# Kernel optimization log

Measured on AMD Instinct MI355X. Metric: run time of the kernel, lower is better.

## Reference

```python
import jax, jax.numpy as jnp
import numpy as np

_EPS = 1e-6
_ZCA_EPS = 1e-5
NEG_SLOPE_ATTN = 0.2   # LeakyReLU inside score_mlp
NEG_SLOPE_FFN = 0.1    # VNLinearLeakyReLU negative_slope


def _safe_norm(x, axis, keepdims=False):
    # norm with zero-gradient at exactly-zero vectors (matches torch subgradient)
    sq = jnp.sum(x * x, axis=axis, keepdims=keepdims)
    safe = jnp.where(sq == 0, 1.0, sq)
    return jnp.sqrt(safe) * (sq > 0)


def vn_linear(W, x):
    # W: (out, in); x: (B, C_in, 3, N) -> (B, C_out, 3, N)
    return jnp.einsum('oi,bivn->bovn', W, x)


def zca_layernorm(x, gamma):
    # x: (B, C, 3, N); whiten the 3D vector components per batch element
    B, C = x.shape[0], x.shape[1]
    xf = x.reshape(B, C, 3, -1).transpose(0, 2, 1, 3).reshape(B, 3, -1)
    xf = xf.astype(jnp.float32)
    mu = xf.mean(axis=-1, keepdims=True)
    xc = xf - mu
    M = xc.shape[-1]
    cov = (xc @ xc.transpose(0, 2, 1)) / (float(M) + _EPS)  # (B,3,3)
    cov = cov + _ZCA_EPS * jnp.eye(3, dtype=cov.dtype)[None]
    w, V = jnp.linalg.eigh(cov)
    w = jnp.maximum(w, _ZCA_EPS)
    Wm = (V * jax.lax.rsqrt(w)[:, None, :]) @ V.transpose(0, 2, 1)  # (B,3,3)
    xw = Wm @ xc
    xw = xw.reshape(B, 3, C, -1).transpose(0, 2, 1, 3).reshape(x.shape).astype(x.dtype)
    return xw * gamma[None, :, None, None]


def cwsa_attention(x, pos, Wq, Wk, Wv, Wo, W1, b1, W2, b2):
    q = vn_linear(Wq, x)  # (B,C,3,N)
    k = vn_linear(Wk, x)
    v = vn_linear(Wv, x)
    qk = q.transpose(0, 3, 1, 2)  # (B,N,C,3)
    kk = k.transpose(0, 3, 1, 2)
    vv = v.transpose(0, 3, 1, 2)
    rel = qk[:, :, None, :, :] - kk[:, None, :, :, :]      # (B,N,N,C,3)
    rel_norm = _safe_norm(rel, axis=-1)                    # (B,N,N,C)
    rel_mean = rel_norm.mean(axis=-1, keepdims=True)       # (B,N,N,1)
    rel_pos = pos[:, :, None, :] - pos[:, None, :, :]      # (B,N,N,3)
    rel_pos_norm = _safe_norm(rel_pos, axis=-1, keepdims=True)  # (B,N,N,1)
    score_in = jnp.concatenate([rel_mean, rel_pos_norm], axis=-1)  # (B,N,N,2)
    h = jax.nn.leaky_relu(score_in @ W1.T + b1, NEG_SLOPE_ATTN)
    scores = h @ W2.T + b2                                  # (B,N,N,C)
    attn = jax.nn.softmax(scores, axis=2)                   # softmax over keys j
    out = jnp.einsum('bijk,bjkd->bikd', attn, vv)           # (B,N,C,3)
    out = out.transpose(0, 2, 3, 1)                         # (B,C,3,N)
    return vn_linear(Wo, out)


def vn_leaky_relu(p, d, ns):
    # p, d: (B, C, 3, N)
    dot = jnp.sum(p * d, axis=2, keepdims=True)
    dsq = jnp.sum(d * d, axis=2, keepdims=True)
    mask = (dot >= 0).astype(p.dtype)
    proj = p - (dot / (dsq + _EPS)) * d
    return ns * p + (1.0 - ns) * (mask * p + (1.0 - mask) * proj)


def ffn(x, Wfeat, Wdir, Wffn2):
    p = vn_linear(Wfeat, x)
    d = vn_linear(Wdir, x)
    h = vn_leaky_relu(p, d, NEG_SLOPE_FFN)
    return vn_linear(Wffn2, h)


def setup_inputs() -> dict:
    key = jax.random.key(0)
    ks = jax.random.split(key, 16)
    B, C, N = 2, 128, 256
    hidden, ratio = 64, 2
    sC = 1.0 / np.sqrt(C)
    inp = {
        'x': jax.random.normal(ks[0], (B, C, 3, N), dtype=jnp.float32),
        'pos': jax.random.normal(ks[1], (B, N, 3), dtype=jnp.float32),
        'Wq': jax.random.normal(ks[2], (C, C), dtype=jnp.float32) * sC,
        'Wk': jax.random.normal(ks[3], (C, C), dtype=jnp.float32) * sC,
        'Wv': jax.random.normal(ks[4], (C, C), dtype=jnp.float32) * sC,
        'Wo': jax.random.normal(ks[5], (C, C), dtype=jnp.float32) * sC,
        'W1': jax.random.normal(ks[6], (hidden, 2), dtype=jnp.float32) * (1.0 / np.sqrt(2.0)),
        'b1': jnp.zeros((hidden,), dtype=jnp.float32),
        'W2': jax.random.normal(ks[7], (C, hidden), dtype=jnp.float32) * (1.0 / np.sqrt(hidden)),
        'b2': jnp.zeros((C,), dtype=jnp.float32),
        'gamma1': jnp.ones((C,), dtype=jnp.float32),
        'Wfeat': jax.random.normal(ks[8], (C * ratio, C), dtype=jnp.float32) * sC,
        'Wdir': jax.random.normal(ks[9], (C * ratio, C), dtype=jnp.float32) * sC,
        'Wffn2': jax.random.normal(ks[10], (C, C * ratio), dtype=jnp.float32) * (1.0 / np.sqrt(C * ratio)),
        'gamma2': jnp.ones((C,), dtype=jnp.float32),
    }
    return inp


def reference(x, pos, Wq, Wk, Wv, Wo, W1, b1, W2, b2, gamma1, Wfeat, Wdir, Wffn2, gamma2):
    a = cwsa_attention(x, pos, Wq, Wk, Wv, Wo, W1, b1, W2, b2)
    x1 = zca_layernorm(x + a, gamma1)
    f = ffn(x1, Wfeat, Wdir, Wffn2)
    return zca_layernorm(x1 + f, gamma2)
```

## Files before the change

### kernel.cpp

```cpp
#include <hip/hip_runtime.h>
#include <math.h>

#define BB 2
#define CC 128
#define NN 256
#define HH 64
#define CHX 256
#define COLS 768
#define NEG_ATTN 0.2f
#define NEG_FFN 0.1f

typedef __attribute__((ext_vector_type(8))) short short8b;
typedef __attribute__((ext_vector_type(4))) float f32x4;

__device__ __forceinline__ unsigned bf16rne(float x) {
  unsigned u = __float_as_uint(x);
  return (u + 0x7fffu + ((u >> 16) & 1u)) >> 16;
}

__global__ __launch_bounds__(256) void k_qkv(
    const float* __restrict__ x, const float* __restrict__ Wq,
    const float* __restrict__ Wk, const float* __restrict__ Wv,
    float* __restrict__ q_t, float* __restrict__ k_nat, float* __restrict__ v_t)
{
  const int ct = blockIdx.x, b = blockIdx.z;
  const int which = blockIdx.y >> 1, cohalf = blockIdx.y & 1;
  const int col0 = ct * 32, co0 = cohalf * 64;
  const int t = threadIdx.x;
  __shared__ __align__(16) float xt[CC][32];
  __shared__ float Wl[64][33];
  const float* xb = x + (size_t)b * CC * COLS;
  for (int idx = t; idx < CC * 32; idx += 256) {
    int r = idx >> 5, cc = idx & 31;
    xt[r][cc] = xb[r * COLS + col0 + cc];
  }
  const float* W = (which == 0) ? Wq : ((which == 1) ? Wk : Wv);
  const int cop = t >> 3;
  const int colq = t & 7;
  float acc[2][4];
#pragma unroll
  for (int r = 0; r < 2; r++)
#pragma unroll
    for (int k = 0; k < 4; k++) acc[r][k] = 0.f;
  for (int cu = 0; cu < 4; cu++) {
    __syncthreads();
    for (int idx = t; idx < 64 * 32; idx += 256) {
      int row = idx >> 5, ci = idx & 31;
      Wl[row][ci] = W[(size_t)(co0 + row) * CC + cu * 32 + ci];
    }
    __syncthreads();
#pragma unroll 8
    for (int ci = 0; ci < 32; ci++) {
      float w0 = Wl[cop * 2][ci], w1 = Wl[cop * 2 + 1][ci];
      const float4 xv = *(reinterpret_cast<const float4*>(xt[cu * 32 + ci]) + colq);
      acc[0][0] = fmaf(w0, xv.x, acc[0][0]); acc[0][1] = fmaf(w0, xv.y, acc[0][1]);
      acc[0][2] = fmaf(w0, xv.z, acc[0][2]); acc[0][3] = fmaf(w0, xv.w, acc[0][3]);
      acc[1][0] = fmaf(w1, xv.x, acc[1][0]); acc[1][1] = fmaf(w1, xv.y, acc[1][1]);
      acc[1][2] = fmaf(w1, xv.z, acc[1][2]); acc[1][3] = fmaf(w1, xv.w, acc[1][3]);
    }
  }
#pragma unroll
  for (int r = 0; r < 2; r++) {
    const int co_g = co0 + cop * 2 + r;
    if (which == 1) {
      float4 o = {acc[r][0], acc[r][1], acc[r][2], acc[r][3]};
      *reinterpret_cast<float4*>(&k_nat[(size_t)(b * CC + co_g) * COLS + col0 + colq * 4]) = o;
    } else {
#pragma unroll
      for (int k = 0; k < 4; k++) {
        int col = col0 + colq * 4 + k;
        int v = col >> 8, n = col & 255;
        if (which == 0) q_t[((size_t)(b * NN + n) * CC + co_g) * 3 + v] = acc[r][k];
        else            v_t[((size_t)(b * NN + n) * 3 + v) * CC + co_g] = acc[r][k];
      }
    }
  }
}

__global__ __launch_bounds__(256) void k_rel(
    const float* __restrict__ q_t, const float* __restrict__ k_nat,
    const float* __restrict__ pos, float* __restrict__ rm_all,
    float* __restrict__ rp_all)
{
  const int i = blockIdx.x, b = blockIdx.y;
  const int t = threadIdx.x;
  __shared__ float qv[CC * 3];
  for (int idx = t; idx < CC * 3; idx += 256)
    qv[idx] = q_t[(size_t)(b * NN + i) * CC * 3 + idx];
  __syncthreads();
  const int j = t;
  const float* kb = k_nat + (size_t)b * CC * COLS;
  float p0 = 0.f, p1 = 0.f, p2 = 0.f, p3 = 0.f;
  for (int c = 0; c < CC; c += 4) {
    float kx0 = kb[(c + 0) * COLS + j], ky0 = kb[(c + 0) * COLS + 256 + j], kz0 = kb[(c + 0) * COLS + 512 + j];
    float kx1 = kb[(c + 1) * COLS + j], ky1 = kb[(c + 1) * COLS + 256 + j], kz1 = kb[(c + 1) * COLS + 512 + j];
    float kx2 = kb[(c + 2) * COLS + j], ky2 = kb[(c + 2) * COLS + 256 + j], kz2 = kb[(c + 2) * COLS + 512 + j];
    float kx3 = kb[(c + 3) * COLS + j], ky3 = kb[(c + 3) * COLS + 256 + j], kz3 = kb[(c + 3) * COLS + 512 + j];
    float dx, dy, dz, sq;
    dx = kx0 - qv[(c + 0) * 3]; dy = ky0 - qv[(c + 0) * 3 + 1]; dz = kz0 - qv[(c + 0) * 3 + 2];
    sq = dx * dx + dy * dy + dz * dz; p0 += (sq > 0.f) ? sqrtf(sq) : 0.f;
    dx = kx1 - qv[(c + 1) * 3]; dy = ky1 - qv[(c + 1) * 3 + 1]; dz = kz1 - qv[(c + 1) * 3 + 2];
    sq = dx * dx + dy * dy + dz * dz; p1 += (sq > 0.f) ? sqrtf(sq) : 0.f;
    dx = kx2 - qv[(c + 2) * 3]; dy = ky2 - qv[(c + 2) * 3 + 1]; dz = kz2 - qv[(c + 2) * 3 + 2];
    sq = dx * dx + dy * dy + dz * dz; p2 += (sq > 0.f) ? sqrtf(sq) : 0.f;
    dx = kx3 - qv[(c + 3) * 3]; dy = ky3 - qv[(c + 3) * 3 + 1]; dz = kz3 - qv[(c + 3) * 3 + 2];
    sq = dx * dx + dy * dy + dz * dz; p3 += (sq > 0.f) ? sqrtf(sq) : 0.f;
  }
  rm_all[(size_t)(b * NN + i) * NN + j] = ((p0 + p1) + (p2 + p3)) * (1.f / 128.f);
  float dx = pos[(b * NN + i) * 3 + 0] - pos[(b * NN + j) * 3 + 0];
  float dy = pos[(b * NN + i) * 3 + 1] - pos[(b * NN + j) * 3 + 1];
  float dz = pos[(b * NN + i) * 3 + 2] - pos[(b * NN + j) * 3 + 2];
  float sq = dx * dx + dy * dy + dz * dz;
  rp_all[(size_t)(b * NN + i) * NN + j] = (sq > 0.f) ? sqrtf(sq) : 0.f;
}

__global__ __launch_bounds__(256, 4) void k_attn(
    const float* __restrict__ rm_all, const float* __restrict__ rp_all,
    const float* __restrict__ v_t, const float* __restrict__ W1,
    const float* __restrict__ b1, const float* __restrict__ W2,
    float* __restrict__ a_nat)
{
  const int i = blockIdx.x, chalf = blockIdx.y, b = blockIdx.z;
  const int t = threadIdx.x;
  __shared__ __align__(16) short hh_s[64 * 64];
  __shared__ __align__(16) short w2_s[64 * 64];
  __shared__ float sc_s[64 * 65];
  __shared__ float rm_s[NN], rp_s[NN];

  rm_s[t] = rm_all[(size_t)(b * NN + i) * NN + t];
  rp_s[t] = rp_all[(size_t)(b * NN + i) * NN + t];
  {
    const int cl = t >> 2, h0 = (t & 3) * 16;
    const float* wrow = W2 + (size_t)(chalf * 64 + cl) * HH + h0;
#pragma unroll
    for (int e = 0; e < 8; e++) {
      unsigned lo = bf16rne(wrow[2 * e]);
      unsigned hi = bf16rne(wrow[2 * e + 1]);
      int didx = (cl * 32 + (h0 >> 1) + e) ^ ((cl & 7) << 2);
      ((unsigned*)w2_s)[didx] = lo | (hi << 16);
    }
  }
  const int h2 = (t & 31) * 2, jgrp = t >> 5;
  const float4 w1v = *reinterpret_cast<const float4*>(W1 + 2 * h2);
  const float c0 = b1[h2], c1 = b1[h2 + 1];
  __syncthreads();

  auto phase2 = [&](int q) {
#pragma unroll
    for (int jj = 0; jj < 8; jj++) {
      int jl = jgrp * 8 + jj;
      int jg = q * 64 + jl;
      float rmv = rm_s[jg], rpv = rp_s[jg];
      float g0 = fmaf(w1v.x, rmv, fmaf(w1v.y, rpv, c0));
      float g1 = fmaf(w1v.z, rmv, fmaf(w1v.w, rpv, c1));
      g0 = (g0 >= 0.f) ? g0 : NEG_ATTN * g0;
      g1 = (g1 >= 0.f) ? g1 : NEG_ATTN * g1;
      int didx = (jl * 32 + (h2 >> 1)) ^ ((jl & 7) << 2);
      ((unsigned*)hh_s)[didx] = bf16rne(g0) | (bf16rne(g1) << 16);
    }
  };

  phase2(0);
  __syncthreads();

  const int lane = t & 63, wv = t >> 6;
  const int g8 = (lane >> 4) * 8;
  const int cdx = wv * 16 + (lane & 15);
  const short8b bfr0 = *reinterpret_cast<const short8b*>(&w2_s[(cdx * 64 + g8) ^ ((cdx & 7) << 3)]);
  const short8b bfr1 = *reinterpret_cast<const short8b*>(&w2_s[(cdx * 64 + 32 + g8) ^ ((cdx & 7) << 3)]);

  const int cl = lane;
  const int par = wv;
  const int vc = chalf * 64 + cl;
  float l = 0.f, a0 = 0.f, a1 = 0.f, a2 = 0.f;

  for (int q = 0; q < 4; q++) {
#pragma unroll
    for (int jt = 0; jt < 4; jt++) {
      int jr = jt * 16 + (lane & 15);
      short8b af0 = *reinterpret_cast<const short8b*>(&hh_s[(jr * 64 + g8) ^ ((jr & 7) << 3)]);
      short8b af1 = *reinterpret_cast<const short8b*>(&hh_s[(jr * 64 + 32 + g8) ^ ((jr & 7) << 3)]);
      f32x4 acc = {0.f, 0.f, 0.f, 0.f};
      acc = __builtin_amdgcn_mfma_f32_16x16x32_bf16(af0, bfr0, acc, 0, 0, 0);
      acc = __builtin_amdgcn_mfma_f32_16x16x32_bf16(af1, bfr1, acc, 0, 0, 0);
      int row0 = jt * 16 + (lane >> 4) * 4;
      int ccol = wv * 16 + (lane & 15);
#pragma unroll
      for (int r = 0; r < 4; r++) sc_s[(row0 + r) * 65 + ccol] = acc[r];
    }
    __syncthreads();
#pragma unroll
    for (int jj = 0; jj < 16; jj++) {
      int jl = jj * 4 + par;
      int jg = q * 64 + jl;
      float s = sc_s[jl * 65 + cl];
      const float* vb = v_t + ((size_t)(b * NN + jg) * 3) * CC + vc;
      float v0 = vb[0], v1 = vb[CC], v2 = vb[2 * CC];
      float p = __expf(s);
      l += p;
      a0 = fmaf(p, v0, a0);
      a1 = fmaf(p, v1, a1);
      a2 = fmaf(p, v2, a2);
    }
    if (q < 3) phase2(q + 1);
    __syncthreads();
  }

  float* mrg = sc_s;
  if (par != 0) {
    float* mp = mrg + (cl * 3 + (par - 1)) * 4;
    mp[0] = l; mp[1] = a0; mp[2] = a1; mp[3] = a2;
  }
  __syncthreads();
  if (par == 0) {
    float L = l, A0 = a0, A1 = a1, A2 = a2;
#pragma unroll
    for (int q = 0; q < 3; q++) {
      const float* mp = mrg + (cl * 3 + q) * 4;
      L += mp[0]; A0 += mp[1]; A1 += mp[2]; A2 += mp[3];
    }
    float inv = 1.f / L;
    float* ap = a_nat + (size_t)(b * CC + vc) * COLS + i;
    ap[0] = A0 * inv; ap[256] = A1 * inv; ap[512] = A2 * inv;
  }
}

__global__ __launch_bounds__(256) void k_wo_res(
    const float* __restrict__ a_nat, const float* __restrict__ Wo,
    const float* __restrict__ x, float* __restrict__ y1)
{
  const int ct = blockIdx.x, cohalf = blockIdx.y, b = blockIdx.z;
  const int col0 = ct * 16, co0 = cohalf * 64;
  const int t = threadIdx.x;
  __shared__ __align__(16) float at[CC][16];
  __shared__ float Wl[64][33];
  const float* ab = a_nat + (size_t)b * CC * COLS;
  for (int idx = t; idx < CC * 16; idx += 256) {
    int r = idx >> 4, cc = idx & 15;
    at[r][cc] = ab[r * COLS + col0 + cc];
  }
  const int cop = t >> 3, colp = t & 7;
  float acc[2][2] = {{0.f, 0.f}, {0.f, 0.f}};
  for (int cu = 0; cu < 4; cu++) {
    __syncthreads();
    for (int idx = t; idx < 64 * 32; idx += 256) {
      int row = idx >> 5, ci = idx & 31;
      Wl[row][ci] = Wo[(size_t)(co0 + row) * CC + cu * 32 + ci];
    }
    __syncthreads();
#pragma unroll 8
    for (int ci = 0; ci < 32; ci++) {
      float w0 = Wl[cop * 2][ci], w1 = Wl[cop * 2 + 1][ci];
      const float2 xv = *(reinterpret_cast<const float2*>(at[cu * 32 + ci]) + colp);
      acc[0][0] = fmaf(w0, xv.x, acc[0][0]); acc[0][1] = fmaf(w0, xv.y, acc[0][1]);
      acc[1][0] = fmaf(w1, xv.x, acc[1][0]); acc[1][1] = fmaf(w1, xv.y, acc[1][1]);
    }
  }
#pragma unroll
  for (int r = 0; r < 2; r++) {
    const size_t base = (size_t)(b * CC + co0 + cop * 2 + r) * COLS + col0 + colp * 2;
    y1[base]     = x[base]     + acc[r][0];
    y1[base + 1] = x[base + 1] + acc[r][1];
  }
}

__global__ __launch_bounds__(1024) void k_stats(
    const float* __restrict__ y, float* __restrict__ stats)
{
  const int b = blockIdx.x;
  const float* yb = y + (size_t)b * CC * COLS;
  const int t = threadIdx.x;
  float v9[9];
#pragma unroll
  for (int k = 0; k < 9; k++) v9[k] = 0.f;
  for (int e = 0; e < 32; e++) {
    int idx = e * 1024 + t;
    int cidx = idx >> 8, n = idx & 255;
    const float* row = yb + cidx * COLS + n;
    float v0 = row[0], v1 = row[256], v2 = row[512];
    v9[0] += v0; v9[1] += v1; v9[2] += v2;
    v9[3] += v0 * v0; v9[4] += v0 * v1; v9[5] += v0 * v2;
    v9[6] += v1 * v1; v9[7] += v1 * v2; v9[8] += v2 * v2;
  }
#pragma unroll
  for (int off = 32; off >= 1; off >>= 1)
#pragma unroll
    for (int k = 0; k < 9; k++) v9[k] += __shfl_down(v9[k], off);
  __shared__ float red[16][9];
  const int wid = t >> 6, lane = t & 63;
  if (lane == 0)
#pragma unroll
    for (int k = 0; k < 9; k++) red[wid][k] = v9[k];
  __syncthreads();
  if (t == 0) {
    float tot[9];
#pragma unroll
    for (int k = 0; k < 9; k++) tot[k] = 0.f;
    for (int w = 0; w < 16; w++)
#pragma unroll
      for (int k = 0; k < 9; k++) tot[k] += red[w][k];
    const float M = (float)(CC * NN);
    float mu0 = tot[0] / M, mu1 = tot[1] / M, mu2 = tot[2] / M;
    float A[3][3];
    A[0][0] = (tot[3] - M * mu0 * mu0) / M + 1e-5f;
    A[0][1] = A[1][0] = (tot[4] - M * mu0 * mu1) / M;
    A[0][2] = A[2][0] = (tot[5] - M * mu0 * mu2) / M;
    A[1][1] = (tot[6] - M * mu1 * mu1) / M + 1e-5f;
    A[1][2] = A[2][1] = (tot[7] - M * mu1 * mu2) / M;
    A[2][2] = (tot[8] - M * mu2 * mu2) / M + 1e-5f;
    float V[3][3] = {{1.f, 0.f, 0.f}, {0.f, 1.f, 0.f}, {0.f, 0.f, 1.f}};
    for (int sweep = 0; sweep < 10; sweep++) {
      for (int pi = 0; pi < 3; pi++) {
        const int p = (pi == 2) ? 1 : 0;
        const int q = (pi == 0) ? 1 : 2;
        float apq = A[p][q];
        if (fabsf(apq) < 1e-30f) continue;
        float theta = (A[q][q] - A[p][p]) / (2.f * apq);
        float tt = 1.f / (fabsf(theta) + sqrtf(theta * theta + 1.f));
        if (theta < 0.f) tt = -tt;
        float cr = 1.f / sqrtf(tt * tt + 1.f);
        float sr = tt * cr;
        float app = A[p][p], aqq = A[q][q];
        A[p][p] = app - tt * apq;
        A[q][q] = aqq + tt * apq;
        A[p][q] = A[q][p] = 0.f;
        const int r = 3 - p - q;
        float arp = A[r][p], arq = A[r][q];
        A[r][p] = A[p][r] = cr * arp - sr * arq;
        A[r][q] = A[q][r] = sr * arp + cr * arq;
        for (int rr = 0; rr < 3; rr++) {
          float vrp = V[rr][p], vrq = V[rr][q];
          V[rr][p] = cr * vrp - sr * vrq;
          V[rr][q] = sr * vrp + cr * vrq;
        }
      }
    }
    float rs[3];
#pragma unroll
    for (int k = 0; k < 3; k++) rs[k] = rsqrtf(fmaxf(A[k][k], 1e-5f));
    float* st = stats + b * 12;
    st[0] = mu0; st[1] = mu1; st[2] = mu2;
    for (int u = 0; u < 3; u++)
      for (int v = 0; v < 3; v++) {
        float acc = 0.f;
        for (int k = 0; k < 3; k++) acc += V[u][k] * rs[k] * V[v][k];
        st[3 + u * 3 + v] = acc;
      }
  }
}

__global__ __launch_bounds__(256) void k_ffn1(
    const float* __restrict__ y1, const float* __restrict__ stats,
    const float* __restrict__ gamma, const float* __restrict__ Wfeat,
    const float* __restrict__ Wdir, float* __restrict__ hout)
{
  const int nt = blockIdx.x, cs = blockIdx.y, b = blockIdx.z;
  const int n0 = nt * 8, co0 = cs * 32;
  const int t = threadIdx.x;
  __shared__ float xt[CC][24];
  __shared__ float Wfl[32][33], Wdl[32][33];
  const float* yb = y1 + (size_t)b * CC * COLS;
  const float* st = stats + b * 12;
  for (int idx = t; idx < CC * 8; idx += 256) {
    int ci = idx >> 3, nn = idx & 7;
    const float* row = yb + ci * COLS + n0 + nn;
    float d0 = row[0] - st[0], d1 = row[256] - st[1], d2 = row[512] - st[2];
    float g = gamma[ci];
    xt[ci][nn]      = g * (st[3] * d0 + st[4] * d1 + st[5] * d2);
    xt[ci][8 + nn]  = g * (st[6] * d0 + st[7] * d1 + st[8] * d2);
    xt[ci][16 + nn] = g * (st[9] * d0 + st[10] * d1 + st[11] * d2);
  }
  const int co = t >> 3, nn = t & 7;
  float p[3] = {0.f, 0.f, 0.f}, d[3] = {0.f, 0.f, 0.f};
  for (int cu = 0; cu < 4; cu++) {
    __syncthreads();
    for (int idx = t; idx < 2048; idx += 256) {
      int row = (idx & 1023) >> 5, ci = idx & 31;
      if (idx < 1024) Wfl[row][ci] = Wfeat[(size_t)(co0 + row) * CC + cu * 32 + ci];
      else            Wdl[row][ci] = Wdir[(size_t)(co0 + row) * CC + cu * 32 + ci];
    }
    __syncthreads();
#pragma unroll 8
    for (int ci = 0; ci < 32; ci++) {
      float wf = Wfl[co][ci], wd = Wdl[co][ci];
      const float* xr = xt[cu * 32 + ci];
      float x0 = xr[nn], x1 = xr[8 + nn], x2 = xr[16 + nn];
      p[0] = fmaf(wf, x0, p[0]); p[1] = fmaf(wf, x1, p[1]); p[2] = fmaf(wf, x2, p[2]);
      d[0] = fmaf(wd, x0, d[0]); d[1] = fmaf(wd, x1, d[1]); d[2] = fmaf(wd, x2, d[2]);
    }
  }
  float dot = p[0] * d[0] + p[1] * d[1] + p[2] * d[2];
  float dsq = d[0] * d[0] + d[1] * d[1] + d[2] * d[2];
  float coef = (dot >= 0.f) ? 0.f : (1.f - NEG_FFN) * dot / (dsq + 1e-6f);
  float* hb = hout + (size_t)(b * CHX + co0 + co) * COLS;
#pragma unroll
  for (int v = 0; v < 3; v++)
    hb[v * 256 + n0 + nn] = p[v] - coef * d[v];
}

__global__ __launch_bounds__(256) void k_ffn2(
    const float* __restrict__ h, const float* __restrict__ Wffn2,
    const float* __restrict__ y1, const float* __restrict__ stats,
    const float* __restrict__ gamma, float* __restrict__ x2)
{
  const int ct = blockIdx.x, cohalf = blockIdx.y, b = blockIdx.z;
  const int col0 = ct * 16, co0 = cohalf * 64;
  const int t = threadIdx.x;
  __shared__ __align__(16) float ht[CHX][16];
  __shared__ float Wl[64][33];
  const float* hb = h + (size_t)b * CHX * COLS;
  for (int idx = t; idx < CHX * 16; idx += 256) {
    int r = idx >> 4, cc = idx & 15;
    ht[r][cc] = hb[r * COLS + col0 + cc];
  }
  const int cop = t >> 3, colp = t & 7;
  float acc[2][2] = {{0.f, 0.f}, {0.f, 0.f}};
  for (int cu = 0; cu < 8; cu++) {
    __syncthreads();
    for (int idx = t; idx < 64 * 32; idx += 256) {
      int row = idx >> 5, ci = idx & 31;
      Wl[row][ci] = Wffn2[(size_t)(co0 + row) * CHX + cu * 32 + ci];
    }
    __syncthreads();
#pragma unroll 8
    for (int ci = 0; ci < 32; ci++) {
      float w0 = Wl[cop * 2][ci], w1 = Wl[cop * 2 + 1][ci];
      const float2 xv = *(reinterpret_cast<const float2*>(ht[cu * 32 + ci]) + colp);
      acc[0][0] = fmaf(w0, xv.x, acc[0][0]); acc[0][1] = fmaf(w0, xv.y, acc[0][1]);
      acc[1][0] = fmaf(w1, xv.x, acc[1][0]); acc[1][1] = fmaf(w1, xv.y, acc[1][1]);
    }
  }
  const int col_base = col0 + colp * 2;
  const int v = col_base >> 8, n = col_base & 255;
  const float* st = stats + b * 12;
  const float w0 = st[3 + v * 3 + 0], w1 = st[3 + v * 3 + 1], w2 = st[3 + v * 3 + 2];
#pragma unroll
  for (int r = 0; r < 2; r++) {
    const int co_g = co0 + cop * 2 + r;
    const float g = gamma[co_g];
    const float* yr = y1 + (size_t)(b * CC + co_g) * COLS + n;
    const size_t base = (size_t)(b * CC + co_g) * COLS + col_base;
#pragma unroll
    for (int k = 0; k < 2; k++) {
      float d0 = yr[k] - st[0], d1 = yr[256 + k] - st[1], d2 = yr[512 + k] - st[2];
      x2[base + k] = g * (w0 * d0 + w1 * d1 + w2 * d2) + acc[r][k];
    }
  }
}

__global__ __launch_bounds__(256) void k_zca_apply(
    const float* __restrict__ y, const float* __restrict__ stats,
    const float* __restrict__ gamma, float* __restrict__ out)
{
  int idx = blockIdx.x * blockDim.x + threadIdx.x;
  int b = idx >> 15, rem = idx & 32767;
  int cidx = rem >> 8, n = rem & 255;
  const float* st = stats + b * 12;
  const size_t base = (size_t)(b * CC + cidx) * COLS + n;
  float v0 = y[base] - st[0];
  float v1 = y[base + 256] - st[1];
  float v2 = y[base + 512] - st[2];
  float g = gamma[cidx];
  out[base]       = g * (st[3] * v0 + st[4] * v1 + st[5] * v2);
  out[base + 256] = g * (st[6] * v0 + st[7] * v1 + st[8] * v2);
  out[base + 512] = g * (st[9] * v0 + st[10] * v1 + st[11] * v2);
}

extern "C" void kernel_launch(void* const* d_in, const int* in_sizes, int n_in,
                              void* d_out, int out_size, void* d_ws, size_t ws_size,
                              hipStream_t stream)
{
  (void)in_sizes; (void)n_in; (void)out_size; (void)ws_size;
  const float* x      = (const float*)d_in[0];
  const float* pos    = (const float*)d_in[1];
  const float* Wq     = (const float*)d_in[2];
  const float* Wk     = (const float*)d_in[3];
  const float* Wv     = (const float*)d_in[4];
  const float* Wo     = (const float*)d_in[5];
  const float* W1     = (const float*)d_in[6];
  const float* b1     = (const float*)d_in[7];
  const float* W2     = (const float*)d_in[8];
  const float* gamma1 = (const float*)d_in[10];
  const float* Wfeat  = (const float*)d_in[11];
  const float* Wdir   = (const float*)d_in[12];
  const float* Wffn2  = (const float*)d_in[13];
  const float* gamma2 = (const float*)d_in[14];

  float* ws = (float*)d_ws;
  const size_t SZ = (size_t)BB * CC * 3 * NN;
  const size_t RMSZ = (size_t)BB * NN * NN;
  float* q_t    = ws;
  float* k_nat  = ws + SZ;
  float* v_t    = ws + 2 * SZ;
  float* rm_all = ws + 3 * SZ;
  float* rp_all = ws + 3 * SZ + RMSZ;
  float* a_nat  = ws;
  float* y1     = ws + SZ;
  float* hbuf   = ws + 2 * SZ;
  float* x2     = ws;
  float* stats1 = ws + 4 * SZ;
  float* stats2 = ws + 4 * SZ + 64;

  k_qkv<<<dim3(24, 6, BB), 256, 0, stream>>>(x, Wq, Wk, Wv, q_t, k_nat, v_t);
  k_rel<<<dim3(NN, BB), 256, 0, stream>>>(q_t, k_nat, pos, rm_all, rp_all);
  k_attn<<<dim3(NN, 2, BB), 256, 0, stream>>>(rm_all, rp_all, v_t, W1, b1, W2, a_nat);
  k_wo_res<<<dim3(48, 2, BB), 256, 0, stream>>>(a_nat, Wo, x, y1);
  k_stats<<<BB, 1024, 0, stream>>>(y1, stats1);
  k_ffn1<<<dim3(32, 8, BB), 256, 0, stream>>>(y1, stats1, gamma1, Wfeat, Wdir, hbuf);
  k_ffn2<<<dim3(48, 2, BB), 256, 0, stream>>>(hbuf, Wffn2, y1, stats1, gamma1, x2);
  k_stats<<<BB, 1024, 0, stream>>>(x2, stats2);
  k_zca_apply<<<256, 256, 0, stream>>>(x2, stats2, gamma2, (float*)d_out);
}
```

Before: 119.3 us.

## Reuse K across query pairs, consume MFMA scores in registers, split ZCA stats reduction

```diff
diff --git a/kernel.cpp b/kernel.cpp
--- a/kernel.cpp
+++ b/kernel.cpp
@@ -82,36 +82,47 @@
     const float* __restrict__ pos, float* __restrict__ rm_all,
     float* __restrict__ rp_all)
 {
-  const int i = blockIdx.x, b = blockIdx.y;
+  const int i0 = blockIdx.x * 2, b = blockIdx.y;
   const int t = threadIdx.x;
-  __shared__ float qv[CC * 3];
-  for (int idx = t; idx < CC * 3; idx += 256)
-    qv[idx] = q_t[(size_t)(b * NN + i) * CC * 3 + idx];
+  __shared__ float qv[2 * CC * 3];
+  for (int idx = t; idx < 2 * CC * 3; idx += 256)
+    qv[idx] = q_t[(size_t)(b * NN + i0) * CC * 3 + idx];
   __syncthreads();
   const int j = t;
   const float* kb = k_nat + (size_t)b * CC * COLS;
-  float p0 = 0.f, p1 = 0.f, p2 = 0.f, p3 = 0.f;
-  for (int c = 0; c < CC; c += 4) {
-    float kx0 = kb[(c + 0) * COLS + j], ky0 = kb[(c + 0) * COLS + 256 + j], kz0 = kb[(c + 0) * COLS + 512 + j];
+  float a00 = 0.f, a01 = 0.f, a10 = 0.f, a11 = 0.f;
+  for (int c = 0; c < CC; c += 2) {
+    float kx0 = kb[c * COLS + j], ky0 = kb[c * COLS + 256 + j], kz0 = kb[c * COLS + 512 + j];
     float kx1 = kb[(c + 1) * COLS + j], ky1 = kb[(c + 1) * COLS + 256 + j], kz1 = kb[(c + 1) * COLS + 512 + j];
-    float kx2 = kb[(c + 2) * COLS + j], ky2 = kb[(c + 2) * COLS + 256 + j], kz2 = kb[(c + 2) * COLS + 512 + j];
-    float kx3 = kb[(c + 3) * COLS + j], ky3 = kb[(c + 3) * COLS + 256 + j], kz3 = kb[(c + 3) * COLS + 512 + j];
-    float dx, dy, dz, sq;
-    dx = kx0 - qv[(c + 0) * 3]; dy = ky0 - qv[(c + 0) * 3 + 1]; dz = kz0 - qv[(c + 0) * 3 + 2];
-    sq = dx * dx + dy * dy + dz * dz; p0 += (sq > 0.f) ? sqrtf(sq) : 0.f;
-    dx = kx1 - qv[(c + 1) * 3]; dy = ky1 - qv[(c + 1) * 3 + 1]; dz = kz1 - qv[(c + 1) * 3 + 2];
-    sq = dx * dx + dy * dy + dz * dz; p1 += (sq > 0.f) ? sqrtf(sq) : 0.f;
-    dx = kx2 - qv[(c + 2) * 3]; dy = ky2 - qv[(c + 2) * 3 + 1]; dz = kz2 - qv[(c + 2) * 3 + 2];
-    sq = dx * dx + dy * dy + dz * dz; p2 += (sq > 0.f) ? sqrtf(sq) : 0.f;
-    dx = kx3 - qv[(c + 3) * 3]; dy = ky3 - qv[(c + 3) * 3 + 1]; dz = kz3 - qv[(c + 3) * 3 + 2];
-    sq = dx * dx + dy * dy + dz * dz; p3 += (sq > 0.f) ? sqrtf(sq) : 0.f;
-  }
-  rm_all[(size_t)(b * NN + i) * NN + j] = ((p0 + p1) + (p2 + p3)) * (1.f / 128.f);
-  float dx = pos[(b * NN + i) * 3 + 0] - pos[(b * NN + j) * 3 + 0];
-  float dy = pos[(b * NN + i) * 3 + 1] - pos[(b * NN + j) * 3 + 1];
-  float dz = pos[(b * NN + i) * 3 + 2] - pos[(b * NN + j) * 3 + 2];
-  float sq = dx * dx + dy * dy + dz * dz;
-  rp_all[(size_t)(b * NN + i) * NN + j] = (sq > 0.f) ? sqrtf(sq) : 0.f;
+    {
+      float dx = kx0 - qv[c * 3], dy = ky0 - qv[c * 3 + 1], dz = kz0 - qv[c * 3 + 2];
+      float sq = dx * dx + dy * dy + dz * dz;
+      a00 += (sq > 0.f) ? sqrtf(sq) : 0.f;
+      dx = kx1 - qv[(c + 1) * 3]; dy = ky1 - qv[(c + 1) * 3 + 1]; dz = kz1 - qv[(c + 1) * 3 + 2];
+      sq = dx * dx + dy * dy + dz * dz;
+      a01 += (sq > 0.f) ? sqrtf(sq) : 0.f;
+    }
+    {
+      const float* q1 = qv + CC * 3;
+      float dx = kx0 - q1[c * 3], dy = ky0 - q1[c * 3 + 1], dz = kz0 - q1[c * 3 + 2];
+      float sq = dx * dx + dy * dy + dz * dz;
+      a10 += (sq > 0.f) ? sqrtf(sq) : 0.f;
+      dx = kx1 - q1[(c + 1) * 3]; dy = ky1 - q1[(c + 1) * 3 + 1]; dz = kz1 - q1[(c + 1) * 3 + 2];
+      sq = dx * dx + dy * dy + dz * dz;
+      a11 += (sq > 0.f) ? sqrtf(sq) : 0.f;
+    }
+  }
+  rm_all[(size_t)(b * NN + i0) * NN + j]     = (a00 + a01) * (1.f / 128.f);
+  rm_all[(size_t)(b * NN + i0 + 1) * NN + j] = (a10 + a11) * (1.f / 128.f);
+  float pjx = pos[(b * NN + j) * 3], pjy = pos[(b * NN + j) * 3 + 1], pjz = pos[(b * NN + j) * 3 + 2];
+#pragma unroll
+  for (int ii = 0; ii < 2; ii++) {
+    float dx = pos[(b * NN + i0 + ii) * 3] - pjx;
+    float dy = pos[(b * NN + i0 + ii) * 3 + 1] - pjy;
+    float dz = pos[(b * NN + i0 + ii) * 3 + 2] - pjz;
+    float sq = dx * dx + dy * dy + dz * dz;
+    rp_all[(size_t)(b * NN + i0 + ii) * NN + j] = (sq > 0.f) ? sqrtf(sq) : 0.f;
+  }
 }
 
 __global__ __launch_bounds__(256, 4) void k_attn(
@@ -122,10 +133,10 @@
 {
   const int i = blockIdx.x, chalf = blockIdx.y, b = blockIdx.z;
   const int t = threadIdx.x;
-  __shared__ __align__(16) short hh_s[64 * 64];
+  __shared__ __align__(16) short hh_s[2][64 * 64];
   __shared__ __align__(16) short w2_s[64 * 64];
-  __shared__ float sc_s[64 * 65];
   __shared__ float rm_s[NN], rp_s[NN];
+  __shared__ float mrg[64][3][4];
 
   rm_s[t] = rm_all[(size_t)(b * NN + i) * NN + t];
   rp_s[t] = rp_all[(size_t)(b * NN + i) * NN + t];
@@ -143,9 +154,9 @@
   const int h2 = (t & 31) * 2, jgrp = t >> 5;
   const float4 w1v = *reinterpret_cast<const float4*>(W1 + 2 * h2);
   const float c0 = b1[h2], c1 = b1[h2 + 1];
-  __syncthreads();
 
   auto phase2 = [&](int q) {
+    unsigned* dst = (unsigned*)hh_s[q & 1];
 #pragma unroll
     for (int jj = 0; jj < 8; jj++) {
       int jl = jgrp * 8 + jj;
@@ -156,10 +167,11 @@
       g0 = (g0 >= 0.f) ? g0 : NEG_ATTN * g0;
       g1 = (g1 >= 0.f) ? g1 : NEG_ATTN * g1;
       int didx = (jl * 32 + (h2 >> 1)) ^ ((jl & 7) << 2);
-      ((unsigned*)hh_s)[didx] = bf16rne(g0) | (bf16rne(g1) << 16);
+      dst[didx] = bf16rne(g0) | (bf16rne(g1) << 16);
     }
   };
 
+  __syncthreads();
   phase2(0);
   __syncthreads();
 
@@ -169,54 +181,47 @@
   const short8b bfr0 = *reinterpret_cast<const short8b*>(&w2_s[(cdx * 64 + g8) ^ ((cdx & 7) << 3)]);
   const short8b bfr1 = *reinterpret_cast<const short8b*>(&w2_s[(cdx * 64 + 32 + g8) ^ ((cdx & 7) << 3)]);
 
-  const int cl = lane;
-  const int par = wv;
-  const int vc = chalf * 64 + cl;
+  const int vc = chalf * 64 + cdx;
+  const int jg4 = (lane >> 4) * 4;
   float l = 0.f, a0 = 0.f, a1 = 0.f, a2 = 0.f;
 
   for (int q = 0; q < 4; q++) {
+    const short* hb = hh_s[q & 1];
 #pragma unroll
     for (int jt = 0; jt < 4; jt++) {
       int jr = jt * 16 + (lane & 15);
-      short8b af0 = *reinterpret_cast<const short8b*>(&hh_s[(jr * 64 + g8) ^ ((jr & 7) << 3)]);
-      short8b af1 = *reinterpret_cast<const short8b*>(&hh_s[(jr * 64 + 32 + g8) ^ ((jr & 7) << 3)]);
+      short8b af0 = *reinterpret_cast<const short8b*>(&hb[(jr * 64 + g8) ^ ((jr & 7) << 3)]);
+      short8b af1 = *reinterpret_cast<const short8b*>(&hb[(jr * 64 + 32 + g8) ^ ((jr & 7) << 3)]);
       f32x4 acc = {0.f, 0.f, 0.f, 0.f};
       acc = __builtin_amdgcn_mfma_f32_16x16x32_bf16(af0, bfr0, acc, 0, 0, 0);
       acc = __builtin_amdgcn_mfma_f32_16x16x32_bf16(af1, bfr1, acc, 0, 0, 0);
-      int row0 = jt * 16 + (lane >> 4) * 4;
-      int ccol = wv * 16 + (lane & 15);
-#pragma unroll
-      for (int r = 0; r < 4; r++) sc_s[(row0 + r) * 65 + ccol] = acc[r];
-    }
-    __syncthreads();
-#pragma unroll
-    for (int jj = 0; jj < 16; jj++) {
-      int jl = jj * 4 + par;
-      int jg = q * 64 + jl;
-      float s = sc_s[jl * 65 + cl];
-      const float* vb = v_t + ((size_t)(b * NN + jg) * 3) * CC + vc;
-      float v0 = vb[0], v1 = vb[CC], v2 = vb[2 * CC];
-      float p = __expf(s);
-      l += p;
-      a0 = fmaf(p, v0, a0);
-      a1 = fmaf(p, v1, a1);
-      a2 = fmaf(p, v2, a2);
+      const int jbase = q * 64 + jt * 16 + jg4;
+#pragma unroll
+      for (int r = 0; r < 4; r++) {
+        float p = __expf(acc[r]);
+        const float* vb = v_t + ((size_t)(b * NN + jbase + r) * 3) * CC + vc;
+        l += p;
+        a0 = fmaf(p, vb[0], a0);
+        a1 = fmaf(p, vb[CC], a1);
+        a2 = fmaf(p, vb[2 * CC], a2);
+      }
     }
     if (q < 3) phase2(q + 1);
     __syncthreads();
   }
 
-  float* mrg = sc_s;
-  if (par != 0) {
-    float* mp = mrg + (cl * 3 + (par - 1)) * 4;
+  const int g = lane >> 4;
+  const int cslot = cdx;
+  if (g != 0) {
+    float* mp = &mrg[cslot][g - 1][0];
     mp[0] = l; mp[1] = a0; mp[2] = a1; mp[3] = a2;
   }
   __syncthreads();
-  if (par == 0) {
+  if (g == 0) {
     float L = l, A0 = a0, A1 = a1, A2 = a2;
 #pragma unroll
-    for (int q = 0; q < 3; q++) {
-      const float* mp = mrg + (cl * 3 + q) * 4;
+    for (int gg = 0; gg < 3; gg++) {
+      const float* mp = &mrg[cslot][gg][0];
       L += mp[0]; A0 += mp[1]; A1 += mp[2]; A2 += mp[3];
     }
     float inv = 1.f / L;
@@ -264,17 +269,17 @@
   }
 }
 
-__global__ __launch_bounds__(1024) void k_stats(
-    const float* __restrict__ y, float* __restrict__ stats)
-{
-  const int b = blockIdx.x;
+__global__ __launch_bounds__(256) void k_stats1(
+    const float* __restrict__ y, float* __restrict__ partials)
+{
+  const int blk = blockIdx.x, b = blockIdx.y;
   const float* yb = y + (size_t)b * CC * COLS;
-  const int t = threadIdx.x;
   float v9[9];
 #pragma unroll
   for (int k = 0; k < 9; k++) v9[k] = 0.f;
-  for (int e = 0; e < 32; e++) {
-    int idx = e * 1024 + t;
+#pragma unroll
+  for (int e = 0; e < 4; e++) {
+    int idx = blk * 1024 + e * 256 + threadIdx.x;
     int cidx = idx >> 8, n = idx & 255;
     const float* row = yb + cidx * COLS + n;
     float v0 = row[0], v1 = row[256], v2 = row[512];
@@ -286,67 +291,78 @@
   for (int off = 32; off >= 1; off >>= 1)
 #pragma unroll
     for (int k = 0; k < 9; k++) v9[k] += __shfl_down(v9[k], off);
-  __shared__ float red[16][9];
-  const int wid = t >> 6, lane = t & 63;
+  __shared__ float red[4][9];
+  const int wid = threadIdx.x >> 6, lane = threadIdx.x & 63;
   if (lane == 0)
 #pragma unroll
     for (int k = 0; k < 9; k++) red[wid][k] = v9[k];
   __syncthreads();
-  if (t == 0) {
-    float tot[9];
-#pragma unroll
-    for (int k = 0; k < 9; k++) tot[k] = 0.f;
-    for (int w = 0; w < 16; w++)
-#pragma unroll
-      for (int k = 0; k < 9; k++) tot[k] += red[w][k];
-    const float M = (float)(CC * NN);
-    float mu0 = tot[0] / M, mu1 = tot[1] / M, mu2 = tot[2] / M;
-    float A[3][3];
-    A[0][0] = (tot[3] - M * mu0 * mu0) / M + 1e-5f;
-    A[0][1] = A[1][0] = (tot[4] - M * mu0 * mu1) / M;
-    A[0][2] = A[2][0] = (tot[5] - M * mu0 * mu2) / M;
-    A[1][1] = (tot[6] - M * mu1 * mu1) / M + 1e-5f;
-    A[1][2] = A[2][1] = (tot[7] - M * mu1 * mu2) / M;
-    A[2][2] = (tot[8] - M * mu2 * mu2) / M + 1e-5f;
-    float V[3][3] = {{1.f, 0.f, 0.f}, {0.f, 1.f, 0.f}, {0.f, 0.f, 1.f}};
-    for (int sweep = 0; sweep < 10; sweep++) {
-      for (int pi = 0; pi < 3; pi++) {
-        const int p = (pi == 2) ? 1 : 0;
-        const int q = (pi == 0) ? 1 : 2;
-        float apq = A[p][q];
-        if (fabsf(apq) < 1e-30f) continue;
-        float theta = (A[q][q] - A[p][p]) / (2.f * apq);
-        float tt = 1.f / (fabsf(theta) + sqrtf(theta * theta + 1.f));
-        if (theta < 0.f) tt = -tt;
-        float cr = 1.f / sqrtf(tt * tt + 1.f);
-        float sr = tt * cr;
-        float app = A[p][p], aqq = A[q][q];
-        A[p][p] = app - tt * apq;
-        A[q][q] = aqq + tt * apq;
-        A[p][q] = A[q][p] = 0.f;
-        const int r = 3 - p - q;
-        float arp = A[r][p], arq = A[r][q];
-        A[r][p] = A[p][r] = cr * arp - sr * arq;
-        A[r][q] = A[q][r] = sr * arp + cr * arq;
-        for (int rr = 0; rr < 3; rr++) {
-          float vrp = V[rr][p], vrq = V[rr][q];
-          V[rr][p] = cr * vrp - sr * vrq;
-          V[rr][q] = sr * vrp + cr * vrq;
-        }
+  if (threadIdx.x == 0) {
+#pragma unroll
+    for (int k = 0; k < 9; k++)
+      partials[(size_t)(b * 32 + blk) * 9 + k] =
+          ((red[0][k] + red[1][k]) + (red[2][k] + red[3][k]));
+  }
+}
+
+__global__ __launch_bounds__(64) void k_zca_fin(
+    const float* __restrict__ partials, float* __restrict__ stats)
+{
+  const int b = blockIdx.x;
+  if (threadIdx.x != 0) return;
+  float tot[9];
+#pragma unroll
+  for (int k = 0; k < 9; k++) tot[k] = 0.f;
+  for (int p = 0; p < 32; p++)
+#pragma unroll
+    for (int k = 0; k < 9; k++) tot[k] += partials[(size_t)(b * 32 + p) * 9 + k];
+  const float M = (float)(CC * NN);
+  float mu0 = tot[0] / M, mu1 = tot[1] / M, mu2 = tot[2] / M;
+  float A[3][3];
+  A[0][0] = (tot[3] - M * mu0 * mu0) / M + 1e-5f;
+  A[0][1] = A[1][0] = (tot[4] - M * mu0 * mu1) / M;
+  A[0][2] = A[2][0] = (tot[5] - M * mu0 * mu2) / M;
+  A[1][1] = (tot[6] - M * mu1 * mu1) / M + 1e-5f;
+  A[1][2] = A[2][1] = (tot[7] - M * mu1 * mu2) / M;
+  A[2][2] = (tot[8] - M * mu2 * mu2) / M + 1e-5f;
+  float V[3][3] = {{1.f, 0.f, 0.f}, {0.f, 1.f, 0.f}, {0.f, 0.f, 1.f}};
+  for (int sweep = 0; sweep < 10; sweep++) {
+    for (int pi = 0; pi < 3; pi++) {
+      const int p = (pi == 2) ? 1 : 0;
+      const int q = (pi == 0) ? 1 : 2;
+      float apq = A[p][q];
+      if (fabsf(apq) < 1e-30f) continue;
+      float theta = (A[q][q] - A[p][p]) / (2.f * apq);
+      float tt = 1.f / (fabsf(theta) + sqrtf(theta * theta + 1.f));
+      if (theta < 0.f) tt = -tt;
+      float cr = 1.f / sqrtf(tt * tt + 1.f);
+      float sr = tt * cr;
+      float app = A[p][p], aqq = A[q][q];
+      A[p][p] = app - tt * apq;
+      A[q][q] = aqq + tt * apq;
+      A[p][q] = A[q][p] = 0.f;
+      const int r = 3 - p - q;
+      float arp = A[r][p], arq = A[r][q];
+      A[r][p] = A[p][r] = cr * arp - sr * arq;
+      A[r][q] = A[q][r] = sr * arp + cr * arq;
+      for (int rr = 0; rr < 3; rr++) {
+        float vrp = V[rr][p], vrq = V[rr][q];
+        V[rr][p] = cr * vrp - sr * vrq;
+        V[rr][q] = sr * vrp + cr * vrq;
       }
     }
-    float rs[3];
-#pragma unroll
-    for (int k = 0; k < 3; k++) rs[k] = rsqrtf(fmaxf(A[k][k], 1e-5f));
-    float* st = stats + b * 12;
-    st[0] = mu0; st[1] = mu1; st[2] = mu2;
-    for (int u = 0; u < 3; u++)
-      for (int v = 0; v < 3; v++) {
-        float acc = 0.f;
-        for (int k = 0; k < 3; k++) acc += V[u][k] * rs[k] * V[v][k];
-        st[3 + u * 3 + v] = acc;
-      }
-  }
+  }
+  float rs[3];
+#pragma unroll
+  for (int k = 0; k < 3; k++) rs[k] = rsqrtf(fmaxf(A[k][k], 1e-5f));
+  float* st = stats + b * 12;
+  st[0] = mu0; st[1] = mu1; st[2] = mu2;
+  for (int u = 0; u < 3; u++)
+    for (int v = 0; v < 3; v++) {
+      float acc = 0.f;
+      for (int k = 0; k < 3; k++) acc += V[u][k] * rs[k] * V[v][k];
+      st[3 + u * 3 + v] = acc;
+    }
 }
 
 __global__ __launch_bounds__(256) void k_ffn1(
@@ -498,16 +514,19 @@
   float* y1     = ws + SZ;
   float* hbuf   = ws + 2 * SZ;
   float* x2     = ws;
-  float* stats1 = ws + 4 * SZ;
-  float* stats2 = ws + 4 * SZ + 64;
+  float* part   = ws + 4 * SZ;
+  float* stats1 = ws + 4 * SZ + 640;
+  float* stats2 = ws + 4 * SZ + 704;
 
   k_qkv<<<dim3(24, 6, BB), 256, 0, stream>>>(x, Wq, Wk, Wv, q_t, k_nat, v_t);
-  k_rel<<<dim3(NN, BB), 256, 0, stream>>>(q_t, k_nat, pos, rm_all, rp_all);
+  k_rel<<<dim3(NN / 2, BB), 256, 0, stream>>>(q_t, k_nat, pos, rm_all, rp_all);
   k_attn<<<dim3(NN, 2, BB), 256, 0, stream>>>(rm_all, rp_all, v_t, W1, b1, W2, a_nat);
   k_wo_res<<<dim3(48, 2, BB), 256, 0, stream>>>(a_nat, Wo, x, y1);
-  k_stats<<<BB, 1024, 0, stream>>>(y1, stats1);
+  k_stats1<<<dim3(32, BB), 256, 0, stream>>>(y1, part);
+  k_zca_fin<<<BB, 64, 0, stream>>>(part, stats1);
   k_ffn1<<<dim3(32, 8, BB), 256, 0, stream>>>(y1, stats1, gamma1, Wfeat, Wdir, hbuf);
   k_ffn2<<<dim3(48, 2, BB), 256, 0, stream>>>(hbuf, Wffn2, y1, stats1, gamma1, x2);
-  k_stats<<<BB, 1024, 0, stream>>>(x2, stats2);
+  k_stats1<<<dim3(32, BB), 256, 0, stream>>>(x2, part);
+  k_zca_fin<<<BB, 64, 0, stream>>>(part, stats2);
   k_zca_apply<<<256, 256, 0, stream>>>(x2, stats2, gamma2, (float*)d_out);
 }
```

Result: slower. 128.9 us (+8.0%).
